# Optimization experiments

Measured on AMD Instinct MI355X. Metric: run time of the kernel, lower is better.

## Reference

```python
import jax, jax.numpy as jnp
import numpy as np

D_MODEL, D_INNER, D_STATE, HEADDIM, NHEADS, D_CONV, EPS = 2048, 4096, 64, 64, 64, 4, 1e-5
CONV_DIM = D_INNER + 2 * D_STATE  # ngroups=1


def setup_inputs() -> dict:
    key = jax.random.key(0)
    ks = jax.random.split(key, 8)
    return {
        "hidden_states": jax.random.normal(ks[0], (2, 2048, D_MODEL), jnp.float32),
        "rms_weight": jnp.ones((D_MODEL,), jnp.float32),
        "in_proj_w": jax.random.normal(ks[1], (2 * D_INNER + 2 * D_STATE + NHEADS, D_MODEL), jnp.float32) * 0.02,
        "conv_w": jax.random.normal(ks[2], (CONV_DIM, D_CONV), jnp.float32) * 0.2,
        "conv_b": jnp.zeros((CONV_DIM,), jnp.float32),
        "dt_bias": jax.random.normal(ks[3], (NHEADS,), jnp.float32) * 0.5,
        "A_log": jax.random.uniform(ks[4], (NHEADS,), jnp.float32, 0.0, 1.0),
        "D": jnp.ones((NHEADS,), jnp.float32),
        "norm_w": jnp.ones((D_INNER,), jnp.float32),
        "out_proj_w": jax.random.normal(ks[5], (D_MODEL, D_INNER), jnp.float32) * 0.02,
    }


def _rmsnorm(x, w, eps=EPS):
    var = jnp.mean(jnp.square(x), axis=-1, keepdims=True)
    return x * jax.lax.rsqrt(var + eps) * w


def reference(hidden_states, rms_weight, in_proj_w, conv_w, conv_b, dt_bias, A_log, D, norm_w, out_proj_w):
    b, l, _ = hidden_states.shape
    residual = hidden_states
    u = _rmsnorm(hidden_states, rms_weight)
    zxbcdt = jnp.einsum("bld,ed->ble", u, in_proj_w)
    z = zxbcdt[..., :D_INNER]
    xBC = zxbcdt[..., D_INNER:D_INNER + CONV_DIM]
    dt = zxbcdt[..., D_INNER + CONV_DIM:]  # (b, l, h)

    # causal depthwise conv1d over seq
    xBC_t = jnp.transpose(xBC, (0, 2, 1))  # (b, c, l)
    kernel = conv_w[:, None, :]  # (c, 1, k)
    xBC_t = jax.lax.conv_general_dilated(
        xBC_t, kernel, window_strides=(1,), padding=[(D_CONV - 1, 0)],
        feature_group_count=CONV_DIM,
        dimension_numbers=("NCH", "OIH", "NCH"))
    xBC = jax.nn.silu(jnp.transpose(xBC_t, (0, 2, 1)) + conv_b)

    x = xBC[..., :D_INNER].reshape(b, l, NHEADS, HEADDIM)
    B = xBC[..., D_INNER:D_INNER + D_STATE]  # (b, l, n)
    C = xBC[..., D_INNER + D_STATE:]         # (b, l, n)

    dt = jax.nn.softplus(dt + dt_bias)  # (b, l, h)
    A = -jnp.exp(A_log)                 # (h,)
    dA = jnp.exp(dt * A)                # (b, l, h)

    # sequential selective scan over time
    def step(state, inp):
        dA_t, dt_t, x_t, B_t, C_t = inp  # (b,h), (b,h), (b,h,p), (b,n), (b,n)
        state = state * dA_t[:, :, None, None] + jnp.einsum(
            "bh,bhp,bn->bhpn", dt_t, x_t, B_t)
        y_t = jnp.einsum("bhpn,bn->bhp", state, C_t)
        return state, y_t

    xs = (jnp.moveaxis(dA, 1, 0), jnp.moveaxis(dt, 1, 0),
          jnp.moveaxis(x, 1, 0), jnp.moveaxis(B, 1, 0), jnp.moveaxis(C, 1, 0))
    state0 = jnp.zeros((b, NHEADS, HEADDIM, D_STATE), hidden_states.dtype)
    _, ys = jax.lax.scan(step, state0, xs)
    y = jnp.moveaxis(ys, 0, 1)  # (b, l, h, p)
    y = y + D[None, None, :, None] * x
    y = y.reshape(b, l, D_INNER)

    # gated RMSNorm, then output projection
    y = _rmsnorm(y * jax.nn.silu(z), norm_w)
    out = jnp.einsum("ble,de->bld", y, out_proj_w)
    return residual + out
```

## Files before the change

### kernel.cpp

```cpp
#include <hip/hip_runtime.h>
#include <stdint.h>

#define DEV static __device__ __forceinline__

typedef __attribute__((ext_vector_type(8))) __bf16 bf16x8;
typedef __attribute__((ext_vector_type(4))) float f32x4;
typedef __attribute__((ext_vector_type(16))) float f32x16;

DEV float b2f(unsigned short u) {
    union { unsigned int i; float f; } v; v.i = ((unsigned int)u) << 16; return v.f;
}
DEV unsigned short f2b(float f) {
    unsigned int u = __builtin_bit_cast(unsigned int, f);
    unsigned int r = (u + 0x7FFFu + ((u >> 16) & 1u)) >> 16;
    return (unsigned short)r;
}
DEV f32x4 mfma16(bf16x8 a, bf16x8 b, f32x4 c) {
    return __builtin_amdgcn_mfma_f32_16x16x32_bf16(a, b, c, 0, 0, 0);
}
DEV f32x16 mfma32(bf16x8 a, bf16x8 b, f32x16 c) {
    return __builtin_amdgcn_mfma_f32_32x32x16_bf16(a, b, c, 0, 0, 0);
}

DEV void gload16(const void* g, void* l) {
    __builtin_amdgcn_global_load_lds(
        (const __attribute__((address_space(1))) void*)g,
        (__attribute__((address_space(3))) void*)l, 16, 0, 0);
}

__global__ __launch_bounds__(256) void k_cvt(
    const float* __restrict__ src, unsigned short* __restrict__ dst)
{
    long i = ((long)blockIdx.x * 256 + threadIdx.x) * 8;
    float4 a = *(const float4*)(src + i);
    float4 b = *(const float4*)(src + i + 4);
    union { uint4 v; unsigned short s[8]; } o;
    o.s[0] = f2b(a.x); o.s[1] = f2b(a.y); o.s[2] = f2b(a.z); o.s[3] = f2b(a.w);
    o.s[4] = f2b(b.x); o.s[5] = f2b(b.y); o.s[6] = f2b(b.z); o.s[7] = f2b(b.w);
    *(uint4*)(dst + i) = o.v;
}

__global__ __launch_bounds__(256) void k_rmsnorm_in(
    const float* __restrict__ h, const float* __restrict__ w,
    unsigned short* __restrict__ u)
{
    int row = blockIdx.x, t = threadIdx.x;
    const float* hp = h + (long)row * 2048 + t * 8;
    float4 a = *(const float4*)hp;
    float4 b = *(const float4*)(hp + 4);
    float x[8] = {a.x, a.y, a.z, a.w, b.x, b.y, b.z, b.w};
    float ss = 0.f;
#pragma unroll
    for (int i = 0; i < 8; i++) ss += x[i] * x[i];
#pragma unroll
    for (int o = 32; o > 0; o >>= 1) ss += __shfl_down(ss, o);
    __shared__ float red[4];
    if ((t & 63) == 0) red[t >> 6] = ss;
    __syncthreads();
    float tot = red[0] + red[1] + red[2] + red[3];
    float scale = rsqrtf(tot * (1.0f / 2048.0f) + 1e-5f);
    float4 wa = *(const float4*)(w + t * 8);
    float4 wb = *(const float4*)(w + t * 8 + 4);
    float wv[8] = {wa.x, wa.y, wa.z, wa.w, wb.x, wb.y, wb.z, wb.w};
    union { uint4 v; unsigned short s[8]; } ow;
#pragma unroll
    for (int i = 0; i < 8; i++) ow.s[i] = f2b(x[i] * scale * wv[i]);
    *(uint4*)(u + (long)row * 2048 + t * 8) = ow.v;
}

template <int EPI>
__global__ __launch_bounds__(256) void k_gemm_bt(
    const unsigned short* __restrict__ A, const unsigned short* __restrict__ Bm,
    int K, int nvalid, unsigned short* __restrict__ Cb, float* __restrict__ Cf,
    int ldc, const float* __restrict__ Res)
{
    __shared__ __align__(16) unsigned short sA[128 * 64];
    __shared__ __align__(16) unsigned short sB[128 * 64];
    int t = threadIdx.x;
    int w = t >> 6, L = t & 63;

    int flat = blockIdx.y * gridDim.x + blockIdx.x;
    int per = gridDim.x * 8;
    int strip = flat / per;
    int rem = flat - strip * per;
    long m0 = (long)(strip * 8 + (rem & 7)) * 128;
    long n0 = (long)(rem >> 3) * 128;

    int rloc = t >> 3;
    int c16  = t & 7;
    int csw  = c16 ^ (rloc & 7);
    const unsigned short* gAp[4];
    const unsigned short* gBp[4];
#pragma unroll
    for (int i = 0; i < 4; i++) {
        gAp[i] = A + (m0 + i * 32 + rloc) * (long)K + csw * 8;
        long rb = n0 + i * 32 + rloc;
        if (rb >= nvalid) rb = nvalid - 1;
        gBp[i] = Bm + rb * (long)K + csw * 8;
    }
    unsigned short* lA = sA + t * 8;
    unsigned short* lB = sB + t * 8;

    int mw = (w >> 1) * 64, nw = (w & 1) * 64;
    int rowA = mw + (L & 31), rowB = nw + (L & 31);
    int swA = (rowA & 7) << 4, swB = (rowB & 7) << 4;
    int q16 = (L >> 5) * 16;
    const char* pA = (const char*)sA + rowA * 128;
    const char* pB = (const char*)sB + rowB * 128;

    f32x16 acc[2][2];
#pragma unroll
    for (int ti = 0; ti < 2; ti++)
#pragma unroll
        for (int tj = 0; tj < 2; tj++)
#pragma unroll
            for (int r = 0; r < 16; r++) acc[ti][tj][r] = 0.f;

    for (int kt = 0; kt < K; kt += 64) {
#pragma unroll
        for (int i = 0; i < 4; i++) {
            gload16(gAp[i], lA + i * 2048);
            gload16(gBp[i], lB + i * 2048);
            gAp[i] += 64; gBp[i] += 64;
        }
        __syncthreads();
#pragma unroll
        for (int kk = 0; kk < 4; kk++) {
            bf16x8 af[2], bf[2];
#pragma unroll
            for (int ti = 0; ti < 2; ti++)
                af[ti] = *(const bf16x8*)(pA + ti * 4096 + ((q16 + kk * 32) ^ swA));
#pragma unroll
            for (int tj = 0; tj < 2; tj++)
                bf[tj] = *(const bf16x8*)(pB + tj * 4096 + ((q16 + kk * 32) ^ swB));
#pragma unroll
            for (int ti = 0; ti < 2; ti++)
#pragma unroll
                for (int tj = 0; tj < 2; tj++)
                    acc[ti][tj] = mfma32(af[ti], bf[tj], acc[ti][tj]);
        }
        __syncthreads();
    }
    int colL = L & 31;
    int rL = (L >> 5) * 4;
#pragma unroll
    for (int ti = 0; ti < 2; ti++)
#pragma unroll
        for (int tj = 0; tj < 2; tj++) {
            long c = n0 + nw + tj * 32 + colL;
            if (c >= nvalid) continue;
#pragma unroll
            for (int r = 0; r < 16; r++) {
                long row = m0 + mw + ti * 32 + (r & 3) + 8 * (r >> 2) + rL;
                float v = acc[ti][tj][r];
                if (EPI == 0) Cb[row * ldc + c] = f2b(v);
                else          Cf[row * ldc + c] = v + Res[row * ldc + c];
            }
        }
}

__global__ __launch_bounds__(128) void k_conv(
    const unsigned short* __restrict__ zx, const float* __restrict__ cw,
    const float* __restrict__ cb, unsigned short* __restrict__ xbc)
{
    int c = blockIdx.x * 128 + threadIdx.x;
    int b = blockIdx.z;
    int l0 = blockIdx.y * 64;
    float w0 = cw[c * 4 + 0], w1 = cw[c * 4 + 1];
    float w2 = cw[c * 4 + 2], w3 = cw[c * 4 + 3];
    float bias = cb[c];
    const unsigned short* src = zx + ((long)b * 2048) * 8384 + 4096 + c;
    float xm3 = (l0 >= 3) ? b2f(src[(long)(l0 - 3) * 8384]) : 0.f;
    float xm2 = (l0 >= 2) ? b2f(src[(long)(l0 - 2) * 8384]) : 0.f;
    float xm1 = (l0 >= 1) ? b2f(src[(long)(l0 - 1) * 8384]) : 0.f;
    const unsigned short* s2 = src + (long)l0 * 8384;
    unsigned short* dst = xbc + ((long)(b * 2048 + l0)) * 4224 + c;
#pragma unroll 8
    for (int i = 0; i < 64; i++) {
        float xl = b2f(*s2); s2 += 8384;
        float a = xm3 * w0 + xm2 * w1 + xm1 * w2 + xl * w3 + bias;
        a = a / (1.f + expf(-a));
        *dst = f2b(a); dst += 4224;
        xm3 = xm2; xm2 = xm1; xm1 = xl;
    }
}

__global__ __launch_bounds__(256) void k_chunk_state_mfma(
    const unsigned short* __restrict__ xbc, const unsigned short* __restrict__ zxdt,
    const float* __restrict__ dt_bias, const float* __restrict__ A_log,
    unsigned short* __restrict__ Sbuf, float* __restrict__ dAtot)
{
    int blk = blockIdx.x;
    int c = blk & 7, bh = blk >> 3;
    int b = bh >> 6, h = bh & 63;
    int tid = threadIdx.x;
    int w = tid >> 6, L = tid & 63;
    int quad = L >> 4, col = L & 15;
    int rowBlk = (w >> 1) * 32, colBlk = (w & 1) * 32;
    __shared__ __align__(16) unsigned short sXp[64 * 72];
    __shared__ __align__(16) unsigned short sBn[64 * 72];
    __shared__ float sdt[64], sL[64];
    float Ah = expf(A_log[h]);
    float dtb = dt_bias[h];
    f32x4 acc[2][2];
#pragma unroll
    for (int ti = 0; ti < 2; ti++)
#pragma unroll
        for (int tj = 0; tj < 2; tj++) acc[ti][tj] = (f32x4){0.f, 0.f, 0.f, 0.f};
    float sumL = 0.f;

    for (int sub = 0; sub < 4; sub++) {
        int l0 = c * 256 + sub * 64;
        {
            int t = tid >> 2, pc = tid & 3;
            const unsigned short* gX = xbc + (long)(b * 2048 + l0 + t) * 4224 + h * 64 + pc * 16;
            union { uint4 v; unsigned short s[8]; } x0, x1;
            x0.v = *(const uint4*)gX; x1.v = *(const uint4*)(gX + 8);
#pragma unroll
            for (int j = 0; j < 8; j++) {
                sXp[(pc * 16 + j) * 72 + t] = x0.s[j];
                sXp[(pc * 16 + 8 + j) * 72 + t] = x1.s[j];
            }
        }
        if (tid < 64) {
            float raw = b2f(zxdt[((long)(b * 2048 + l0 + tid)) * 8384 + 8320 + h]) + dtb;
            float dtv = (raw > 20.f) ? raw : log1pf(expf(raw));
            float cum = dtv;
#pragma unroll
            for (int off = 1; off < 64; off <<= 1) {
                float v = __shfl_up(cum, off);
                if (tid >= off) cum += v;
            }
            sdt[tid] = dtv;
            sL[tid] = -Ah * cum;
        }
        __syncthreads();
        float Lend = sL[63];
        {
            int t = tid >> 2, nc = tid & 3;
            float wt = sdt[t] * __expf(Lend - sL[t]);
            const unsigned short* gB = xbc + (long)(b * 2048 + l0 + t) * 4224 + 4096 + nc * 16;
            union { uint4 v; unsigned short s[8]; } x0, x1;
            x0.v = *(const uint4*)gB; x1.v = *(const uint4*)(gB + 8);
#pragma unroll
            for (int j = 0; j < 8; j++) {
                sBn[(nc * 16 + j) * 72 + t] = f2b(b2f(x0.s[j]) * wt);
                sBn[(nc * 16 + 8 + j) * 72 + t] = f2b(b2f(x1.s[j]) * wt);
            }
        }
        __syncthreads();
        float e_end = __expf(Lend);
        sumL += Lend;
#pragma unroll
        for (int ti = 0; ti < 2; ti++)
#pragma unroll
            for (int tj = 0; tj < 2; tj++)
#pragma unroll
                for (int r = 0; r < 4; r++) acc[ti][tj][r] *= e_end;
#pragma unroll
        for (int kb = 0; kb < 2; kb++) {
            bf16x8 ax[2], bx[2];
#pragma unroll
            for (int ti = 0; ti < 2; ti++)
                ax[ti] = *(const bf16x8*)(sXp + (rowBlk + ti * 16 + col) * 72 + kb * 32 + quad * 8);
#pragma unroll
            for (int tj = 0; tj < 2; tj++)
                bx[tj] = *(const bf16x8*)(sBn + (colBlk + tj * 16 + col) * 72 + kb * 32 + quad * 8);
#pragma unroll
            for (int ti = 0; ti < 2; ti++)
#pragma unroll
                for (int tj = 0; tj < 2; tj++)
                    acc[ti][tj] = mfma16(ax[ti], bx[tj], acc[ti][tj]);
        }
        __syncthreads();
    }
#pragma unroll
    for (int ti = 0; ti < 2; ti++)
#pragma unroll
        for (int tj = 0; tj < 2; tj++)
#pragma unroll
            for (int r = 0; r < 4; r++) {
                int p = rowBlk + ti * 16 + quad * 4 + r;
                int n = colBlk + tj * 16 + col;
                Sbuf[(long)blk * 4096 + p * 64 + n] = f2b(acc[ti][tj][r]);
            }
    if (tid == 0) dAtot[blk] = __expf(sumL);
}

__global__ __launch_bounds__(256) void k_scan_chunk_mfma(
    const unsigned short* __restrict__ xbc, const unsigned short* __restrict__ zxdt,
    const float* __restrict__ dt_bias, const float* __restrict__ A_log,
    const float* __restrict__ Dv,
    const unsigned short* __restrict__ Sbuf, const float* __restrict__ dAtot,
    unsigned short* __restrict__ yout)
{
    int blk = blockIdx.x;
    int c = blk & 7, bh = blk >> 3;
    int b = bh >> 6, h = bh & 63;
    int tid = threadIdx.x;
    int w = tid >> 6, L = tid & 63;
    int quad = L >> 4, col = L & 15;
    int rowBlk = (w >> 1) * 32, colBlk = (w & 1) * 32;
    __shared__ __align__(16) unsigned short sCm[64 * 72];
    __shared__ __align__(16) unsigned short sBtMs[64 * 72];
    __shared__ __align__(16) unsigned short sXp[64 * 72];
    __shared__ __align__(16) unsigned short sBn[64 * 72];
    __shared__ __align__(16) unsigned short sHb[64 * 72];
    __shared__ float sdt[64], sL[64], sEs[64];
    float Ah = expf(A_log[h]);
    float dtb = dt_bias[h];
    float Dh = Dv[h];

    f32x4 acc_h[2][2];
#pragma unroll
    for (int ti = 0; ti < 2; ti++)
#pragma unroll
        for (int tj = 0; tj < 2; tj++) acc_h[ti][tj] = (f32x4){0.f, 0.f, 0.f, 0.f};
    int sb = bh * 8;
    for (int j = 0; j < c; j++) {
        float d = dAtot[sb + j];
        const unsigned short* Sp = Sbuf + (long)(sb + j) * 4096;
#pragma unroll
        for (int ti = 0; ti < 2; ti++)
#pragma unroll
            for (int tj = 0; tj < 2; tj++)
#pragma unroll
                for (int r = 0; r < 4; r++) {
                    int p = rowBlk + ti * 16 + quad * 4 + r;
                    int n = colBlk + tj * 16 + col;
                    acc_h[ti][tj][r] = acc_h[ti][tj][r] * d + b2f(Sp[p * 64 + n]);
                }
    }

    for (int sub = 0; sub < 4; sub++) {
        int l0 = c * 256 + sub * 64;
        {
            int row = tid >> 2, c4 = tid & 3;
            const unsigned short* gR = xbc + (long)(b * 2048 + l0 + row) * 4224;
            uint4 v0 = *(const uint4*)(gR + 4160 + c4 * 8);
            uint4 v1 = *(const uint4*)(gR + 4160 + (c4 + 4) * 8);
            *(uint4*)(sCm + row * 72 + c4 * 8) = v0;
            *(uint4*)(sCm + row * 72 + (c4 + 4) * 8) = v1;
            uint4 w0 = *(const uint4*)(gR + 4096 + c4 * 8);
            uint4 w1 = *(const uint4*)(gR + 4096 + (c4 + 4) * 8);
            *(uint4*)(sBtMs + row * 72 + c4 * 8) = w0;
            *(uint4*)(sBtMs + row * 72 + (c4 + 4) * 8) = w1;
        }
        {
            int t = tid >> 2, pc = tid & 3;
            const unsigned short* gX = xbc + (long)(b * 2048 + l0 + t) * 4224 + h * 64 + pc * 16;
            union { uint4 v; unsigned short s[8]; } x0, x1;
            x0.v = *(const uint4*)gX; x1.v = *(const uint4*)(gX + 8);
#pragma unroll
            for (int j = 0; j < 8; j++) {
                sXp[(pc * 16 + j) * 72 + t] = x0.s[j];
                sXp[(pc * 16 + 8 + j) * 72 + t] = x1.s[j];
            }
        }
        if (tid < 64) {
            float raw = b2f(zxdt[((long)(b * 2048 + l0 + tid)) * 8384 + 8320 + h]) + dtb;
            float dtv = (raw > 20.f) ? raw : log1pf(expf(raw));
            float cum = dtv;
#pragma unroll
            for (int off = 1; off < 64; off <<= 1) {
                float v = __shfl_up(cum, off);
                if (tid >= off) cum += v;
            }
            sdt[tid] = dtv;
            float l = -Ah * cum;
            sL[tid] = l;
            sEs[tid] = __expf(l);
        }
        __syncthreads();
        float Lend = sL[63];
        {
            int t = tid >> 2, nc = tid & 3;
            float wt = sdt[t] * __expf(Lend - sL[t]);
            const unsigned short* gB = xbc + (long)(b * 2048 + l0 + t) * 4224 + 4096 + nc * 16;
            union { uint4 v; unsigned short s[8]; } x0, x1;
            x0.v = *(const uint4*)gB; x1.v = *(const uint4*)(gB + 8);
#pragma unroll
            for (int j = 0; j < 8; j++) {
                sBn[(nc * 16 + j) * 72 + t] = f2b(b2f(x0.s[j]) * wt);
                sBn[(nc * 16 + 8 + j) * 72 + t] = f2b(b2f(x1.s[j]) * wt);
            }
        }
#pragma unroll
        for (int ti = 0; ti < 2; ti++)
#pragma unroll
            for (int tj = 0; tj < 2; tj++)
#pragma unroll
                for (int r = 0; r < 4; r++) {
                    int p = rowBlk + ti * 16 + quad * 4 + r;
                    int n = colBlk + tj * 16 + col;
                    sHb[p * 72 + n] = f2b(acc_h[ti][tj][r]);
                }
        __syncthreads();
        f32x4 g[2][2];
#pragma unroll
        for (int ti = 0; ti < 2; ti++)
#pragma unroll
            for (int tj = 0; tj < 2; tj++) g[ti][tj] = (f32x4){0.f, 0.f, 0.f, 0.f};
#pragma unroll
        for (int kb = 0; kb < 2; kb++) {
            bf16x8 ac[2], bc[2];
#pragma unroll
            for (int ti = 0; ti < 2; ti++)
                ac[ti] = *(const bf16x8*)(sCm + (rowBlk + ti * 16 + col) * 72 + kb * 32 + quad * 8);
#pragma unroll
            for (int tj = 0; tj < 2; tj++)
                bc[tj] = *(const bf16x8*)(sBtMs + (colBlk + tj * 16 + col) * 72 + kb * 32 + quad * 8);
#pragma unroll
            for (int ti = 0; ti < 2; ti++)
#pragma unroll
                for (int tj = 0; tj < 2; tj++)
                    g[ti][tj] = mfma16(ac[ti], bc[tj], g[ti][tj]);
        }
        __syncthreads();
#pragma unroll
        for (int tj = 0; tj < 2; tj++) {
            int t_idx = colBlk + tj * 16 + col;
            float lt = sL[t_idx], dtt = sdt[t_idx];
#pragma unroll
            for (int ti = 0; ti < 2; ti++)
#pragma unroll
                for (int r = 0; r < 4; r++) {
                    int s_idx = rowBlk + ti * 16 + quad * 4 + r;
                    float m = (t_idx <= s_idx) ? g[ti][tj][r] * dtt * __expf(sL[s_idx] - lt) : 0.f;
                    sBtMs[s_idx * 72 + t_idx] = f2b(m);
                }
        }
        __syncthreads();
        f32x4 yv[2][2];
#pragma unroll
        for (int ti = 0; ti < 2; ti++)
#pragma unroll
            for (int tj = 0; tj < 2; tj++) yv[ti][tj] = (f32x4){0.f, 0.f, 0.f, 0.f};
#pragma unroll
        for (int kb = 0; kb < 2; kb++) {
            bf16x8 am[2], bxp[2];
#pragma unroll
            for (int ti = 0; ti < 2; ti++)
                am[ti] = *(const bf16x8*)(sBtMs + (rowBlk + ti * 16 + col) * 72 + kb * 32 + quad * 8);
#pragma unroll
            for (int tj = 0; tj < 2; tj++)
                bxp[tj] = *(const bf16x8*)(sXp + (colBlk + tj * 16 + col) * 72 + kb * 32 + quad * 8);
#pragma unroll
            for (int ti = 0; ti < 2; ti++)
#pragma unroll
                for (int tj = 0; tj < 2; tj++)
                    yv[ti][tj] = mfma16(am[ti], bxp[tj], yv[ti][tj]);
        }
        float es0 = sEs[rowBlk + col], es1 = sEs[rowBlk + 16 + col];
#pragma unroll
        for (int kb = 0; kb < 2; kb++) {
            bf16x8 acx[2], bhh[2];
#pragma unroll
            for (int ti = 0; ti < 2; ti++) {
                union { bf16x8 v; unsigned short s[8]; } a;
                a.v = *(const bf16x8*)(sCm + (rowBlk + ti * 16 + col) * 72 + kb * 32 + quad * 8);
                float es = ti ? es1 : es0;
#pragma unroll
                for (int j = 0; j < 8; j++) a.s[j] = f2b(b2f(a.s[j]) * es);
                acx[ti] = a.v;
            }
#pragma unroll
            for (int tj = 0; tj < 2; tj++)
                bhh[tj] = *(const bf16x8*)(sHb + (colBlk + tj * 16 + col) * 72 + kb * 32 + quad * 8);
#pragma unroll
            for (int ti = 0; ti < 2; ti++)
#pragma unroll
                for (int tj = 0; tj < 2; tj++)
                    yv[ti][tj] = mfma16(acx[ti], bhh[tj], yv[ti][tj]);
        }
        float e_end = __expf(Lend);
#pragma unroll
        for (int ti = 0; ti < 2; ti++)
#pragma unroll
            for (int tj = 0; tj < 2; tj++)
#pragma unroll
                for (int r = 0; r < 4; r++) acc_h[ti][tj][r] *= e_end;
#pragma unroll
        for (int kb = 0; kb < 2; kb++) {
            bf16x8 ax[2], bn[2];
#pragma unroll
            for (int ti = 0; ti < 2; ti++)
                ax[ti] = *(const bf16x8*)(sXp + (rowBlk + ti * 16 + col) * 72 + kb * 32 + quad * 8);
#pragma unroll
            for (int tj = 0; tj < 2; tj++)
                bn[tj] = *(const bf16x8*)(sBn + (colBlk + tj * 16 + col) * 72 + kb * 32 + quad * 8);
#pragma unroll
            for (int ti = 0; ti < 2; ti++)
#pragma unroll
                for (int tj = 0; tj < 2; tj++)
                    acc_h[ti][tj] = mfma16(ax[ti], bn[tj], acc_h[ti][tj]);
        }
#pragma unroll
        for (int ti = 0; ti < 2; ti++)
#pragma unroll
            for (int tj = 0; tj < 2; tj++)
#pragma unroll
                for (int r = 0; r < 4; r++) {
                    int s_idx = rowBlk + ti * 16 + quad * 4 + r;
                    int p = colBlk + tj * 16 + col;
                    float xv = b2f(sXp[p * 72 + s_idx]);
                    float yo = yv[ti][tj][r] + Dh * xv;
                    yout[((long)(b * 2048 + l0 + s_idx)) * 8384 + 4096 + h * 64 + p] = f2b(yo);
                }
        __syncthreads();
    }
}

__global__ __launch_bounds__(256) void k_gatenorm(
    const unsigned short* __restrict__ zx, const float* __restrict__ nw,
    unsigned short* __restrict__ y2)
{
    int row = blockIdx.x, t = threadIdx.x;
    const unsigned short* zr = zx + (long)row * 8384;
    float v[16]; float ss = 0.f;
#pragma unroll
    for (int i = 0; i < 16; i++) {
        int c = t + i * 256;
        float z = b2f(zr[c]);
        float y = b2f(zr[4096 + c]);
        float g = y * (z / (1.f + expf(-z)));
        v[i] = g; ss += g * g;
    }
#pragma unroll
    for (int o = 32; o > 0; o >>= 1) ss += __shfl_down(ss, o);
    __shared__ float red[4];
    if ((t & 63) == 0) red[t >> 6] = ss;
    __syncthreads();
    float tot = red[0] + red[1] + red[2] + red[3];
    float scale = rsqrtf(tot * (1.0f / 4096.0f) + 1e-5f);
#pragma unroll
    for (int i = 0; i < 16; i++) {
        int c = t + i * 256;
        y2[(long)row * 4096 + c] = f2b(v[i] * scale * nw[c]);
    }
}

extern "C" void kernel_launch(void* const* d_in, const int* in_sizes, int n_in,
                              void* d_out, int out_size, void* d_ws, size_t ws_size,
                              hipStream_t stream)
{
    const float* h    = (const float*)d_in[0];
    const float* rmsw = (const float*)d_in[1];
    const float* w1   = (const float*)d_in[2];
    const float* cw   = (const float*)d_in[3];
    const float* cbp  = (const float*)d_in[4];
    const float* dtb  = (const float*)d_in[5];
    const float* alog = (const float*)d_in[6];
    const float* Dv   = (const float*)d_in[7];
    const float* nw   = (const float*)d_in[8];
    const float* w2   = (const float*)d_in[9];

    char* ws = (char*)d_ws;
    unsigned short* zx    = (unsigned short*)ws;
    unsigned short* w1b   = (unsigned short*)(ws + 68681728L);
    unsigned short* xbc   = (unsigned short*)(ws + 68681728L);
    unsigned short* y2    = (unsigned short*)(ws + 68681728L);
    unsigned short* u     = (unsigned short*)(ws + 103284736L);
    unsigned short* Sbuf  = (unsigned short*)(ws + 103284736L);
    float*          dAt   = (float*)(ws + 111673344L);
    unsigned short* w2b   = (unsigned short*)(ws + 103284736L);
    float* outp = (float*)d_out;

    k_rmsnorm_in<<<4096, 256, 0, stream>>>(h, rmsw, u);
    k_cvt<<<8384, 256, 0, stream>>>(w1, w1b);
    k_gemm_bt<0><<<dim3(66, 32), 256, 0, stream>>>(u, w1b, 2048, 8384, zx, nullptr, 8384, nullptr);
    k_conv<<<dim3(33, 32, 2), 128, 0, stream>>>(zx, cw, cbp, xbc);
    k_chunk_state_mfma<<<1024, 256, 0, stream>>>(xbc, zx, dtb, alog, Sbuf, dAt);
    k_scan_chunk_mfma<<<1024, 256, 0, stream>>>(xbc, zx, dtb, alog, Dv, Sbuf, dAt, zx);
    k_gatenorm<<<4096, 256, 0, stream>>>(zx, nw, y2);
    k_cvt<<<4096, 256, 0, stream>>>(w2, w2b);
    k_gemm_bt<1><<<dim3(16, 32), 256, 0, stream>>>(y2, w2b, 4096, 2048, nullptr, outp, 2048, h);
}
```

Baseline: 552.6 us.

## Add 256x256-tile pipelined MFMA GEMM for input projection main columns

Adds a new 512-thread GEMM kernel with 256x256 output tiles, a 4-stage global_load_lds ring buffer with explicit vmcnt waits, XOR-swizzled LDS layout, s_setprio around the MFMA bursts, and a grid swizzle for L2 locality. The first 8192 output columns of the in_proj GEMM use this kernel, and the remaining 192 columns still go through the old 128-tile kernel in a second launch. The goal is more data reuse per tile and better overlap of loads with MFMA work. The cost is a 128KB LDS footprint, an extra kernel launch, and more register pressure.

```diff
diff --git a/kernel.cpp b/kernel.cpp
--- a/kernel.cpp
+++ b/kernel.cpp
@@ -27,6 +27,10 @@
         (const __attribute__((address_space(1))) void*)g,
         (__attribute__((address_space(3))) void*)l, 16, 0, 0);
 }
+
+#define VM_WAIT8 asm volatile("s_waitcnt vmcnt(8)" ::: "memory")
+#define VM_WAIT4 asm volatile("s_waitcnt vmcnt(4)" ::: "memory")
+#define VM_WAIT0 asm volatile("s_waitcnt vmcnt(0)" ::: "memory")
 
 __global__ __launch_bounds__(256) void k_cvt(
     const float* __restrict__ src, unsigned short* __restrict__ dst)
@@ -66,6 +70,122 @@
 #pragma unroll
     for (int i = 0; i < 8; i++) ow.s[i] = f2b(x[i] * scale * wv[i]);
     *(uint4*)(u + (long)row * 2048 + t * 8) = ow.v;
+}
+
+__global__ __launch_bounds__(512, 2) void k_gemm256(
+    const unsigned short* __restrict__ A, const unsigned short* __restrict__ Bm,
+    int K, unsigned short* __restrict__ Cb, int ldc)
+{
+    __shared__ __align__(16) char sMem[131072];
+    int tid = threadIdx.x;
+    int w = tid >> 6, L = tid & 63;
+
+    int nwg = gridDim.x * gridDim.y;
+    int cpx = nwg >> 3;
+    int fl = blockIdx.y * gridDim.x + blockIdx.x;
+    int swz = (fl & 7) * cpx + (fl >> 3);
+    long m0 = (long)(swz % gridDim.x) * 256;
+    long n0 = (long)(swz / gridDim.x) * 256;
+
+    int rloc = tid >> 2;
+    int csw = (tid & 3) ^ ((tid >> 3) & 3);
+    const unsigned short* gA0 = A + (m0 + rloc) * (long)K + csw * 8;
+    const unsigned short* gA1 = A + (m0 + 128 + rloc) * (long)K + csw * 8;
+    const unsigned short* gB0 = Bm + (n0 + rloc) * (long)K + csw * 8;
+    const unsigned short* gB1 = Bm + (n0 + 128 + rloc) * (long)K + csw * 8;
+    int dA0 = tid * 16, dA1 = 8192 + tid * 16;
+    int dB0 = 16384 + tid * 16, dB1 = 24576 + tid * 16;
+
+    int wr = w >> 2, wc = w & 3;
+    int lr = L & 31, lg = L >> 5;
+    int xr = ((lr >> 1) & 3) << 4;
+    int off0 = (lg << 4) ^ xr;
+    int off1 = (32 | (lg << 4)) ^ xr;
+    int aRow = wr * 8192 + lr * 64;
+    int bRow = 16384 + wc * 4096 + lr * 64;
+
+    f32x16 acc[4][2];
+#pragma unroll
+    for (int mi = 0; mi < 4; mi++)
+#pragma unroll
+        for (int nj = 0; nj < 2; nj++)
+#pragma unroll
+            for (int r = 0; r < 16; r++) acc[mi][nj][r] = 0.f;
+
+#pragma unroll
+    for (int p = 0; p < 3; ++p) {
+        char* db = sMem + p * 32768;
+        gload16(gA0, db + dA0); gload16(gA1, db + dA1);
+        gload16(gB0, db + dB0); gload16(gB1, db + dB1);
+        gA0 += 32; gA1 += 32; gB0 += 32; gB1 += 32;
+    }
+    VM_WAIT8;
+    __builtin_amdgcn_s_barrier();
+
+    int NT = K >> 5;
+    for (int t = 0; t < NT; ++t) {
+        const char* bb = sMem + (t & 3) * 32768;
+        char* db = sMem + ((t + 3) & 3) * 32768;
+        bool stage = (t < NT - 3);
+        if (stage) {
+            gload16(gA0, db + dA0); gA0 += 32;
+            gload16(gA1, db + dA1); gA1 += 32;
+        }
+        {
+            bf16x8 a[4], b[2];
+#pragma unroll
+            for (int mi = 0; mi < 4; mi++)
+                a[mi] = *(const bf16x8*)(bb + aRow + mi * 2048 + off0);
+#pragma unroll
+            for (int nj = 0; nj < 2; nj++)
+                b[nj] = *(const bf16x8*)(bb + bRow + nj * 2048 + off0);
+            __builtin_amdgcn_s_setprio(1);
+#pragma unroll
+            for (int mi = 0; mi < 4; mi++)
+#pragma unroll
+                for (int nj = 0; nj < 2; nj++)
+                    acc[mi][nj] = mfma32(a[mi], b[nj], acc[mi][nj]);
+            __builtin_amdgcn_s_setprio(0);
+        }
+        if (stage) {
+            gload16(gB0, db + dB0); gB0 += 32;
+            gload16(gB1, db + dB1); gB1 += 32;
+        }
+        {
+            bf16x8 a[4], b[2];
+#pragma unroll
+            for (int mi = 0; mi < 4; mi++)
+                a[mi] = *(const bf16x8*)(bb + aRow + mi * 2048 + off1);
+#pragma unroll
+            for (int nj = 0; nj < 2; nj++)
+                b[nj] = *(const bf16x8*)(bb + bRow + nj * 2048 + off1);
+            __builtin_amdgcn_s_setprio(1);
+#pragma unroll
+            for (int mi = 0; mi < 4; mi++)
+#pragma unroll
+                for (int nj = 0; nj < 2; nj++)
+                    acc[mi][nj] = mfma32(a[mi], b[nj], acc[mi][nj]);
+            __builtin_amdgcn_s_setprio(0);
+        }
+        if (t < NT - 3)       { VM_WAIT8; }
+        else if (t == NT - 3) { VM_WAIT4; }
+        else if (t == NT - 2) { VM_WAIT0; }
+        __builtin_amdgcn_s_barrier();
+    }
+
+    int colL = L & 31;
+    int rL = (L >> 5) * 4;
+#pragma unroll
+    for (int mi = 0; mi < 4; mi++)
+#pragma unroll
+        for (int nj = 0; nj < 2; nj++) {
+            long c = n0 + wc * 64 + nj * 32 + colL;
+#pragma unroll
+            for (int r = 0; r < 16; r++) {
+                long row = m0 + wr * 128 + mi * 32 + (r & 3) + 8 * (r >> 2) + rL;
+                Cb[row * ldc + c] = f2b(acc[mi][nj][r]);
+            }
+        }
 }
 
 template <int EPI>
@@ -568,7 +688,9 @@
 
     k_rmsnorm_in<<<4096, 256, 0, stream>>>(h, rmsw, u);
     k_cvt<<<8384, 256, 0, stream>>>(w1, w1b);
-    k_gemm_bt<0><<<dim3(66, 32), 256, 0, stream>>>(u, w1b, 2048, 8384, zx, nullptr, 8384, nullptr);
+    k_gemm256<<<dim3(16, 32), 512, 0, stream>>>(u, w1b, 2048, zx, 8384);
+    k_gemm_bt<0><<<dim3(2, 32), 256, 0, stream>>>(
+        u, w1b + 8192L * 2048, 2048, 192, zx + 8192, nullptr, 8384, nullptr);
     k_conv<<<dim3(33, 32, 2), 128, 0, stream>>>(zx, cw, cbp, xbc);
     k_chunk_state_mfma<<<1024, 256, 0, stream>>>(xbc, zx, dtb, alog, Sbuf, dAt);
     k_scan_chunk_mfma<<<1024, 256, 0, stream>>>(xbc, zx, dtb, alog, Dv, Sbuf, dAt, zx);
```

Result: faster. 531.0 us (-3.9%).

## Use 256x256-tile pipelined MFMA GEMM for bulk of input projection

Applied to the files above, without the earlier changes.

Adds a new 512-thread GEMM kernel with 256x256 output tiles, double-buffered swizzled LDS staging, interleaved global loads and MFMA quadrants with explicit waitcnt/barrier scheduling and setprio. It handles the first 8192 output columns of the input projection, while the old 128-tile kernel covers the remaining 192 columns. The aim is more data reuse per LDS load and better overlap of memory with compute in the largest GEMM. In exchange it uses 128KB of LDS and many accumulator registers, which lowers occupancy, and it adds a second launch for the leftover columns.

```diff
diff --git a/kernel.cpp b/kernel.cpp
--- a/kernel.cpp
+++ b/kernel.cpp
@@ -66,6 +66,136 @@
 #pragma unroll
     for (int i = 0; i < 8; i++) ow.s[i] = f2b(x[i] * scale * wv[i]);
     *(uint4*)(u + (long)row * 2048 + t * 8) = ow.v;
+}
+
+__global__ __launch_bounds__(512, 2) void k_gemm256(
+    const unsigned short* __restrict__ A, const unsigned short* __restrict__ Bm,
+    int K, unsigned short* __restrict__ Cb, int ldc)
+{
+    __shared__ __align__(16) char lds[131072];
+    int tid = threadIdx.x;
+    int w = tid >> 6, l = tid & 63;
+    int NT = K >> 6, NI = K >> 7;
+    long Kb = (long)K * 2;
+
+    int nwg = gridDim.x * gridDim.y;
+    int cpx = nwg >> 3;
+    int fl = blockIdx.y * gridDim.x + blockIdx.x;
+    int swz = (fl & 7) * cpx + (fl >> 3);
+    long m0 = (long)(swz % gridDim.x) * 256;
+    long n0 = (long)(swz / gridDim.x) * 256;
+
+    int rl = tid >> 3;
+    int csw16 = (((tid & 7) ^ (rl & 7)) << 4);
+    const char* pA0 = (const char*)A + (m0 + rl) * Kb + csw16;
+    const char* pA1 = (const char*)A + (m0 + 64 + rl) * Kb + csw16;
+    const char* pB0 = (const char*)Bm + (n0 + rl) * Kb + csw16;
+    const char* pB1 = (const char*)Bm + (n0 + 64 + rl) * Kb + csw16;
+    int ldst = tid * 16;
+
+#define STG(P0, P1, RGN, kt, half) do { if ((kt) < NT) {                      \
+    char* Lr_ = lds + (((kt) & 1) << 16) + (RGN) + ((half) << 14);            \
+    long go_ = (long)(half) * 128 * Kb + (long)(kt) * 128;                    \
+    gload16((P0) + go_, Lr_ + ldst);                                          \
+    gload16((P1) + go_, Lr_ + 8192 + ldst); } } while (0)
+
+    int lq = l >> 4, lr15 = l & 15, key = l & 7;
+    int off0 = ((lq ^ key) << 4);
+    int off1 = (((4 + lq) ^ key) << 4);
+    int aB = ((w >> 2) * 128 + lr15) * 128;
+    int bB = 32768 + (((w & 3) * 64 + lr15) * 128);
+
+    bf16x8 aF[4][2], b0F[2][2], b1F[2][2];
+    f32x4 acc[8][4];
+#pragma unroll
+    for (int s = 0; s < 8; s++)
+#pragma unroll
+        for (int t = 0; t < 4; t++) acc[s][t] = (f32x4){0.f, 0.f, 0.f, 0.f};
+
+#define DS_A(mh, BUF) do {                                                    \
+    const char* ba_ = lds + (BUF) + aB + (mh) * 8192;                         \
+    _Pragma("unroll") for (int s_ = 0; s_ < 4; s_++) {                        \
+        aF[s_][0] = *(const bf16x8*)(ba_ + s_ * 2048 + off0);                 \
+        aF[s_][1] = *(const bf16x8*)(ba_ + s_ * 2048 + off1); } } while (0)
+
+#define DS_B(DST, nh, BUF) do {                                               \
+    const char* bb_ = lds + (BUF) + bB + (nh) * 4096;                         \
+    _Pragma("unroll") for (int t_ = 0; t_ < 2; t_++) {                        \
+        DST[t_][0] = *(const bf16x8*)(bb_ + t_ * 2048 + off0);                \
+        DST[t_][1] = *(const bf16x8*)(bb_ + t_ * 2048 + off1); } } while (0)
+
+#define MQ(mh, nh, BF) do {                                                   \
+    __builtin_amdgcn_s_setprio(1);                                            \
+    _Pragma("unroll") for (int kk_ = 0; kk_ < 2; kk_++)                       \
+    _Pragma("unroll") for (int s_ = 0; s_ < 4; s_++)                          \
+    _Pragma("unroll") for (int t_ = 0; t_ < 2; t_++)                          \
+        acc[(mh) * 4 + s_][(nh) * 2 + t_] =                                   \
+            mfma16(aF[s_][kk_], BF[t_][kk_], acc[(mh) * 4 + s_][(nh) * 2 + t_]); \
+    __builtin_amdgcn_s_setprio(0); } while (0)
+
+#define BAR __builtin_amdgcn_s_barrier()
+#define LG0 do { asm volatile("s_waitcnt lgkmcnt(0)" ::: "memory");           \
+                 __builtin_amdgcn_sched_barrier(0); } while (0)
+
+    STG(pA0, pA1, 0,     0, 0);
+    STG(pA0, pA1, 0,     0, 1);
+    STG(pB0, pB1, 32768, 0, 0);
+    STG(pB0, pB1, 32768, 0, 1);
+    STG(pB0, pB1, 32768, 1, 0);
+    STG(pB0, pB1, 32768, 1, 1);
+    STG(pA0, pA1, 0,     1, 0);
+    asm volatile("s_waitcnt vmcnt(6)" ::: "memory");
+    BAR;
+
+    for (int it = 0; it < NI; ++it) {
+        int k1 = 2 * it + 1, k2 = 2 * it + 2, k3 = 2 * it + 3;
+        DS_A(0, 0); DS_B(b0F, 0, 0);
+        STG(pA0, pA1, 0, k1, 1);
+        BAR; LG0; MQ(0, 0, b0F); BAR;
+        DS_B(b1F, 1, 0);
+        BAR; LG0; MQ(0, 1, b1F); BAR;
+        DS_A(1, 0);
+        STG(pB0, pB1, 32768, k2, 0);
+        BAR; LG0; MQ(1, 1, b1F); BAR;
+        STG(pB0, pB1, 32768, k2, 1);
+        BAR; MQ(1, 0, b0F);
+        if (it == NI - 1) { asm volatile("s_waitcnt vmcnt(0)" ::: "memory"); }
+        else              { asm volatile("s_waitcnt vmcnt(4)" ::: "memory"); }
+        BAR;
+        DS_A(0, 65536); DS_B(b0F, 0, 65536);
+        STG(pA0, pA1, 0, k2, 0);
+        BAR; LG0; MQ(0, 0, b0F); BAR;
+        DS_B(b1F, 1, 65536);
+        STG(pA0, pA1, 0, k2, 1);
+        BAR; LG0; MQ(0, 1, b1F); BAR;
+        DS_A(1, 65536);
+        STG(pB0, pB1, 32768, k3, 0);
+        BAR; LG0; MQ(1, 1, b1F); BAR;
+        STG(pB0, pB1, 32768, k3, 1);
+        STG(pA0, pA1, 0, k3, 0);
+        BAR; MQ(1, 0, b0F);
+        if (it < NI - 1) { asm volatile("s_waitcnt vmcnt(6)" ::: "memory"); }
+        BAR;
+    }
+
+    int colb = (w & 3) * 64 + lr15;
+    int rowb = (w >> 2) * 128 + lq * 4;
+#pragma unroll
+    for (int s = 0; s < 8; s++)
+#pragma unroll
+        for (int t = 0; t < 4; t++) {
+            long col = n0 + colb + t * 16;
+            long row = m0 + rowb + s * 16;
+#pragma unroll
+            for (int r = 0; r < 4; r++)
+                Cb[(row + r) * ldc + col] = f2b(acc[s][t][r]);
+        }
+#undef STG
+#undef DS_A
+#undef DS_B
+#undef MQ
+#undef BAR
+#undef LG0
 }
 
 template <int EPI>
@@ -568,7 +698,9 @@
 
     k_rmsnorm_in<<<4096, 256, 0, stream>>>(h, rmsw, u);
     k_cvt<<<8384, 256, 0, stream>>>(w1, w1b);
-    k_gemm_bt<0><<<dim3(66, 32), 256, 0, stream>>>(u, w1b, 2048, 8384, zx, nullptr, 8384, nullptr);
+    k_gemm256<<<dim3(16, 32), 512, 0, stream>>>(u, w1b, 2048, zx, 8384);
+    k_gemm_bt<0><<<dim3(2, 32), 256, 0, stream>>>(
+        u, w1b + 8192L * 2048, 2048, 192, zx + 8192, nullptr, 8384, nullptr);
     k_conv<<<dim3(33, 32, 2), 128, 0, stream>>>(zx, cw, cbp, xbc);
     k_chunk_state_mfma<<<1024, 256, 0, stream>>>(xbc, zx, dtb, alog, Sbuf, dAt);
     k_scan_chunk_mfma<<<1024, 256, 0, stream>>>(xbc, zx, dtb, alog, Dv, Sbuf, dAt, zx);
```

New measurement: 514.1 us. 7.0% less time.
